# Optimization experiments

Hardware: AMD Instinct MI355X
Metric: run time of the kernel (lower is better)

## Reference

```python
import jax, jax.numpy as jnp
import numpy as np

H = 512      # LSTM hidden size (hard-coded in BiLstm)
ATT = 20     # attention size
EPS = 1e-5


def _ln(x, gamma, beta):
    mu = x.mean(-1, keepdims=True)
    var = x.var(-1, keepdims=True)
    return (x - mu) / jnp.sqrt(var + EPS) * gamma + beta


def _bn(x, gamma, beta):
    # BatchNorm1d in training mode: x [B, C, T], stats over (batch, time)
    mu = x.mean((0, 2), keepdims=True)
    var = x.var((0, 2), keepdims=True)
    return (x - mu) / jnp.sqrt(var + EPS) * gamma[None, :, None] + beta[None, :, None]


def _lstm_dir(x_seq, w_ih, w_hh, g_gamma, g_beta, c_gamma, c_beta, reverse):
    # x_seq: [T, B, in] ; w_ih: [4H, in] ; w_hh: [4H, H]
    T, B, _ = x_seq.shape
    xp = jnp.einsum('tbi,gi->tbg', x_seq, w_ih)  # precompute input projections [T,B,4H]
    gg = g_gamma.reshape(4, H)
    gb = g_beta.reshape(4, H)

    def step(carry, xt):
        h, c = carry
        pre = xt + h @ w_hh.T                    # [B, 4H]
        pre = _ln(pre.reshape(B, 4, H), gg, gb)  # per-gate LayerNorm
        i, f, g, o = pre[:, 0], pre[:, 1], pre[:, 2], pre[:, 3]
        c = jax.nn.sigmoid(f) * c + jax.nn.sigmoid(i) * jnp.tanh(g)
        h = jax.nn.sigmoid(o) * jnp.tanh(_ln(c, c_gamma, c_beta))
        return (h, c), h

    init = (jnp.zeros((B, H), x_seq.dtype), jnp.zeros((B, H), x_seq.dtype))
    _, hs = jax.lax.scan(step, init, xp, reverse=reverse)
    return hs  # [T, B, H], time-ordered


def _bilstm_layer(x_seq, w_ih, w_hh, gg, gb, cg, cb):
    fwd = _lstm_dir(x_seq, w_ih[0], w_hh[0], gg[0], gb[0], cg[0], cb[0], False)
    bwd = _lstm_dir(x_seq, w_ih[1], w_hh[1], gg[1], gb[1], cg[1], cb[1], True)
    return jnp.concatenate([fwd, bwd], axis=-1)  # [T, B, 2H]


def setup_inputs() -> dict:
    key = jax.random.key(0)
    ks = jax.random.split(key, 12)
    B, T, V = 32, 512, 128
    d = {}
    d['x'] = jax.random.normal(ks[0], (B, T, V), jnp.float32)
    # BatchNorm params
    d['bn1_gamma'] = jnp.ones((V,), jnp.float32)
    d['bn1_beta'] = jnp.zeros((V,), jnp.float32)
    d['bn2_gamma'] = jnp.ones((2 * H,), jnp.float32)
    d['bn2_beta'] = jnp.zeros((2 * H,), jnp.float32)
    # Layer 0 (input V), layer 1 (input 2H); 2 directions stacked on axis 0
    d['w_ih0'] = jax.random.normal(ks[1], (2, 4 * H, V), jnp.float32) * 0.05
    d['w_hh0'] = jax.random.normal(ks[2], (2, 4 * H, H), jnp.float32) * 0.05
    d['g_gamma0'] = jnp.ones((2, 4 * H), jnp.float32)
    d['g_beta0'] = jnp.zeros((2, 4 * H), jnp.float32)
    d['c_gamma0'] = jnp.ones((2, H), jnp.float32)
    d['c_beta0'] = jnp.zeros((2, H), jnp.float32)
    d['w_ih1'] = jax.random.normal(ks[3], (2, 4 * H, 2 * H), jnp.float32) * 0.05
    d['w_hh1'] = jax.random.normal(ks[4], (2, 4 * H, H), jnp.float32) * 0.05
    d['g_gamma1'] = jnp.ones((2, 4 * H), jnp.float32)
    d['g_beta1'] = jnp.zeros((2, 4 * H), jnp.float32)
    d['c_gamma1'] = jnp.ones((2, H), jnp.float32)
    d['c_beta1'] = jnp.zeros((2, H), jnp.float32)
    # Attention params
    d['w_omega'] = jax.random.normal(ks[5], (2 * H, ATT), jnp.float32) * 0.05
    d['b_omega'] = jax.random.normal(ks[6], (ATT,), jnp.float32) * 0.05
    d['u_omega'] = jax.random.normal(ks[7], (ATT,), jnp.float32) * 0.05
    return d


def reference(x, bn1_gamma, bn1_beta, bn2_gamma, bn2_beta,
              w_ih0, w_hh0, g_gamma0, g_beta0, c_gamma0, c_beta0,
              w_ih1, w_hh1, g_gamma1, g_beta1, c_gamma1, c_beta1,
              w_omega, b_omega, u_omega):
    # x: [B, T, V]; dropout layers are identity (eval)
    h = jnp.transpose(x, (0, 2, 1))              # [B, V, T]
    h = _bn(h, bn1_gamma, bn1_beta)
    h = jnp.transpose(h, (2, 0, 1))              # [T, B, V]
    h = _bilstm_layer(h, w_ih0, w_hh0, g_gamma0, g_beta0, c_gamma0, c_beta0)
    h = _bilstm_layer(h, w_ih1, w_hh1, g_gamma1, g_beta1, c_gamma1, c_beta1)
    h = jnp.transpose(h, (1, 2, 0))              # [B, 2H, T]
    h = _bn(h, bn2_gamma, bn2_beta)
    h = jnp.transpose(h, (0, 2, 1))              # [B, T, 2H]
    # Additive attention pooling
    v = jnp.tanh(h @ w_omega + b_omega)          # [B, T, ATT]
    vu = v @ u_omega                             # [B, T]
    alphas = jax.nn.softmax(vu, axis=1)
    out = jnp.sum(h * alphas[..., None], axis=1)  # [B, 2H]
    return out
```

## Files before the change

kernel.cpp:

```cpp
#include <hip/hip_runtime.h>
#include <hip/hip_bf16.h>

#define LN_EPS 1e-5f

typedef __attribute__((ext_vector_type(4))) float    f32x4;
typedef __attribute__((ext_vector_type(8))) short    s16x8;
typedef __attribute__((ext_vector_type(8))) _Float16 f16x8;
typedef __attribute__((ext_vector_type(4))) unsigned u32x4;

__device__ __forceinline__ float sigmoidf_(float x){ return 1.0f/(1.0f+expf(-x)); }

__device__ __forceinline__ float fsig(float x){
  return 1.0f/(1.0f + __expf(-x));
}
__device__ __forceinline__ float ftanh(float x){
  float xx = fminf(fmaxf(x, -15.f), 15.f);
  float e = __expf(2.f*xx);
  return (e - 1.f)/(e + 1.f);
}

__device__ __forceinline__ short bf16_hi_bits(float f){
  __hip_bfloat16 h = __float2bfloat16(f);
  return *reinterpret_cast<short*>(&h);
}
__device__ __forceinline__ float bf16_hi_val(float f){
  return __bfloat162float(__float2bfloat16(f));
}

__device__ __forceinline__ float agent_load_f(const float* p){
  return __hip_atomic_load((float*)p, __ATOMIC_RELAXED, __HIP_MEMORY_SCOPE_AGENT);
}
__device__ __forceinline__ void agent_store_f(float* p, float v){
  __hip_atomic_store(p, v, __ATOMIC_RELAXED, __HIP_MEMORY_SCOPE_AGENT);
}

__global__ void k_bn1_stats(const float* __restrict__ x, float* __restrict__ stats){
  int tid = threadIdx.x;
  int cg = tid >> 3, ro = tid & 7;
  int c4 = cg * 4;
  float s[4] = {0,0,0,0}, q[4] = {0,0,0,0};
  int rbase = blockIdx.x * 64;
  for (int i = 0; i < 8; ++i){
    int row = rbase + i*8 + ro;
    f32x4 v = *(const f32x4*)(x + (size_t)row*128 + c4);
    #pragma unroll
    for (int e=0;e<4;e++){ s[e]+=v[e]; q[e]+=v[e]*v[e]; }
  }
  #pragma unroll
  for (int o=1;o<8;o<<=1){
    #pragma unroll
    for (int e=0;e<4;e++){ s[e]+=__shfl_xor(s[e],o); q[e]+=__shfl_xor(q[e],o); }
  }
  if (ro==0){
    #pragma unroll
    for (int e=0;e<4;e++){
      atomicAdd(&stats[c4+e], s[e]);
      atomicAdd(&stats[128+c4+e], q[e]);
    }
  }
}

__global__ void k_bn1_fin(const float* __restrict__ stats, const float* __restrict__ gamma,
                          const float* __restrict__ beta, float* __restrict__ ss){
  int c = threadIdx.x;
  if (c < 128){
    float N = 16384.0f;
    float mean = stats[c]/N;
    float var  = stats[128+c]/N - mean*mean;
    float scale = gamma[c] * rsqrtf(var + LN_EPS);
    ss[c] = scale;
    ss[128+c] = beta[c] - mean*scale;
  }
}

__global__ void k_cvt_split(const float* __restrict__ s, __hip_bfloat16* __restrict__ hi,
                            __hip_bfloat16* __restrict__ lo, int n){
  for (int i = blockIdx.x*blockDim.x + threadIdx.x; i < n; i += gridDim.x*blockDim.x){
    float v = s[i];
    __hip_bfloat16 h = __float2bfloat16(v);
    hi[i] = h;
    lo[i] = __float2bfloat16(v - __bfloat162float(h));
  }
}

__global__ void k_pack_whh(const float* __restrict__ whh, _Float16* __restrict__ wpk){
  size_t i = (size_t)blockIdx.x*256 + threadIdx.x;
  int k = (int)(i & 511);
  size_t ci = i >> 9;
  int col = (int)(ci & 2047);
  int dirr = (int)(ci >> 11);
  int gate = col >> 9, cig = col & 511, c16 = cig >> 4, lc = cig & 15;
  int kt = k >> 5, ksub = k & 31, hi = ksub >> 3, j = ksub & 7;
  size_t dst = ((((size_t)(dirr*4+gate)*16 + kt)*32 + c16)*64 + (hi*16+lc))*8 + j;
  wpk[dst] = (_Float16)whh[i];
}

__global__ __launch_bounds__(256) void gemm_split(const float* __restrict__ A,
                                                  const __hip_bfloat16* __restrict__ Bhi,
                                                  const __hip_bfloat16* __restrict__ Blo,
                                                  _Float16* __restrict__ C,
                                                  int M, int N, int K,
                                                  int a_mode, const float* __restrict__ ss){
  __shared__ __align__(16) __hip_bfloat16 Ah[128*32];
  __shared__ __align__(16) __hip_bfloat16 Al[128*32];
  __shared__ __align__(16) __hip_bfloat16 Bh[128*32];
  __shared__ __align__(16) __hip_bfloat16 Bl[128*32];
  int n0 = blockIdx.x * 128, m0 = blockIdx.y * 128;
  int tid = threadIdx.x, lane = tid & 63, wave = tid >> 6;
  int wm = wave >> 1, wn = wave & 1;
  f32x4 acc[4][4] = {};
  int r = tid >> 2, sseg = tid & 3;
  for (int kt = 0; kt < K; kt += 32){
    #pragma unroll
    for (int half = 0; half < 2; ++half){
      int m = m0 + half*64 + r;
      const float* src;
      if (a_mode){
        int t = m >> 5, b = m & 31;
        src = A + ((size_t)(b*512 + t))*128 + kt + sseg*8;
      } else {
        src = A + (size_t)m*K + kt + sseg*8;
      }
      f32x4 v0 = *(const f32x4*)src;
      f32x4 v1 = *(const f32x4*)(src + 4);
      s16x8 vh, vl;
      #pragma unroll
      for (int e=0;e<4;e++){
        float f0 = v0[e], f1 = v1[e];
        if (a_mode){
          int k = kt + sseg*8;
          f0 = f0*ss[k+e]   + ss[128+k+e];
          f1 = f1*ss[k+4+e] + ss[128+k+4+e];
        }
        float h0 = bf16_hi_val(f0), h1 = bf16_hi_val(f1);
        vh[e]   = bf16_hi_bits(f0); vl[e]   = bf16_hi_bits(f0 - h0);
        vh[4+e] = bf16_hi_bits(f1); vl[4+e] = bf16_hi_bits(f1 - h1);
      }
      *(s16x8*)&Ah[(half*64+r)*32 + sseg*8] = vh;
      *(s16x8*)&Al[(half*64+r)*32 + sseg*8] = vl;
      u32x4 bh = *(const u32x4*)(Bhi + (size_t)(n0 + half*64 + r)*K + kt + sseg*8);
      u32x4 bl = *(const u32x4*)(Blo + (size_t)(n0 + half*64 + r)*K + kt + sseg*8);
      *(u32x4*)&Bh[(half*64+r)*32 + sseg*8] = bh;
      *(u32x4*)&Bl[(half*64+r)*32 + sseg*8] = bl;
    }
    __syncthreads();
    s16x8 afh[4], afl[4], bfh[4], bfl[4];
    int k8 = (lane >> 4) * 8;
    int ra = wm*64 + (lane & 15), rb = wn*64 + (lane & 15);
    #pragma unroll
    for (int mi=0;mi<4;mi++){
      afh[mi] = *(const s16x8*)&Ah[(ra + mi*16)*32 + k8];
      afl[mi] = *(const s16x8*)&Al[(ra + mi*16)*32 + k8];
    }
    #pragma unroll
    for (int ni=0;ni<4;ni++){
      bfh[ni] = *(const s16x8*)&Bh[(rb + ni*16)*32 + k8];
      bfl[ni] = *(const s16x8*)&Bl[(rb + ni*16)*32 + k8];
    }
    #pragma unroll
    for (int mi=0;mi<4;mi++)
      #pragma unroll
      for (int ni=0;ni<4;ni++){
        acc[mi][ni] = __builtin_amdgcn_mfma_f32_16x16x32_bf16(afh[mi], bfh[ni], acc[mi][ni], 0, 0, 0);
        acc[mi][ni] = __builtin_amdgcn_mfma_f32_16x16x32_bf16(afl[mi], bfh[ni], acc[mi][ni], 0, 0, 0);
        acc[mi][ni] = __builtin_amdgcn_mfma_f32_16x16x32_bf16(afh[mi], bfl[ni], acc[mi][ni], 0, 0, 0);
      }
    __syncthreads();
  }
  #pragma unroll
  for (int mi=0;mi<4;mi++)
    #pragma unroll
    for (int ni=0;ni<4;ni++){
      int col  = n0 + wn*64 + ni*16 + (lane & 15);
      int row0 = m0 + wm*64 + mi*16 + (lane >> 4)*4;
      #pragma unroll
      for (int rr=0;rr<4;rr++)
        C[(size_t)(row0+rr)*N + col] = (_Float16)acc[mi][ni][rr];
    }
}

#define CHUNK 516

__global__ __launch_bounds__(512, 1) void lstm_fast(
    const _Float16* __restrict__ xp,
    const _Float16* __restrict__ wpk,
    const float* __restrict__ gg, const float* __restrict__ gb,
    const float* __restrict__ cgam, const float* __restrict__ cbet,
    float* __restrict__ out,
    float* __restrict__ tf,
    unsigned* __restrict__ flags)
{
  int blk = blockIdx.x;
  int sub = blk & 15;
  int bq = blk >> 4;
  int dir = sub >> 3, gate = (sub >> 1) & 3, half = sub & 1;
  int tid = threadIdx.x, lane = tid & 63, wv = tid >> 6;
  int b0 = bq * 2;
  int grp = bq*2 + dir;
  int blkbase = (bq << 4) | (dir << 3);
  int own_sub = gate*2 + half;

  __shared__ __align__(16) _Float16 hfrag[16*64*8];
  __shared__ float c_s[2][512];
  __shared__ float red[8][2][2];
  __shared__ float redc[8][2][2];
  __shared__ float lnstat[8][2];

  for (int i = tid; i < 16*64*8; i += 512) hfrag[i] = (_Float16)0.f;
  for (int i = tid; i < 2*512;  i += 512) c_s[i>>9][i&511] = 0.f;
  __syncthreads();

  int j = tid;
  float g0s = gg[dir*2048 + j],        g0b = gb[dir*2048 + j];
  float g1s = gg[dir*2048 + 512 + j],  g1b = gb[dir*2048 + 512 + j];
  float g2s = gg[dir*2048 + 1024 + j], g2b = gb[dir*2048 + 1024 + j];
  float g3s = gg[dir*2048 + 1536 + j], g3b = gb[dir*2048 + 1536 + j];
  float cgv = cgam[dir*512 + j],       cbv = cbet[dir*512 + j];

  const _Float16* wbase = wpk + (size_t)(dir*4 + gate) * (16*32*64*8);
  int c16a = half*16 + wv*2, c16b = c16a + 1;
  f16x8 wA[16], wB[16];
  #pragma unroll
  for (int kt = 0; kt < 16; ++kt){
    wA[kt] = *(const f16x8*)&wbase[(((size_t)kt*32 + c16a)*64 + lane)*8];
    wB[kt] = *(const f16x8*)&wbase[(((size_t)kt*32 + c16b)*64 + lane)*8];
  }

  for (int t = 0; t < 512; ++t){
    asm volatile("" : "+v"(wA[0]), "+v"(wA[1]), "+v"(wA[2]), "+v"(wA[3]),
                      "+v"(wA[4]), "+v"(wA[5]), "+v"(wA[6]), "+v"(wA[7]));
    asm volatile("" : "+v"(wA[8]), "+v"(wA[9]), "+v"(wA[10]), "+v"(wA[11]),
                      "+v"(wA[12]), "+v"(wA[13]), "+v"(wA[14]), "+v"(wA[15]));
    asm volatile("" : "+v"(wB[0]), "+v"(wB[1]), "+v"(wB[2]), "+v"(wB[3]),
                      "+v"(wB[4]), "+v"(wB[5]), "+v"(wB[6]), "+v"(wB[7]));
    asm volatile("" : "+v"(wB[8]), "+v"(wB[9]), "+v"(wB[10]), "+v"(wB[11]),
                      "+v"(wB[12]), "+v"(wB[13]), "+v"(wB[14]), "+v"(wB[15]));
    int pos = dir ? (511 - t) : t;
    int buf = t & 1;
    float xv0[2], xv1[2];
    if (lane < 16){
      const _Float16* xb = xp + (size_t)(pos*32 + b0)*4096 + dir*2048 + gate*512 + half*256;
      #pragma unroll
      for (int r = 0; r < 2; ++r){
        xv0[r] = (float)xb[(size_t)r*4096 + (wv*2)*16 + lane];
        xv1[r] = (float)xb[(size_t)r*4096 + (wv*2)*16 + lane + 16];
      }
    }
    f32x4 acc0 = {}, acc1 = {};
    #pragma unroll
    for (int kt = 0; kt < 16; ++kt){
      f16x8 afrag = *(const f16x8*)&hfrag[(kt*64 + lane)*8];
      acc0 = __builtin_amdgcn_mfma_f32_16x16x32_f16(afrag, wA[kt], acc0, 0, 0, 0);
      acc1 = __builtin_amdgcn_mfma_f32_16x16x32_f16(afrag, wB[kt], acc1, 0, 0, 0);
    }
    float* chk = tf + ((size_t)(grp*2 + buf)*8 + own_sub)*CHUNK;
    float s[2] = {0,0}, q[2] = {0,0};
    if (lane < 16){
      int cA = (wv*2)*16 + lane, cB = cA + 16;
      #pragma unroll
      for (int r = 0; r < 2; ++r){
        float v0 = acc0[r] + xv0[r];
        float v1 = acc1[r] + xv1[r];
        agent_store_f(chk + r*256 + cA, v0);
        agent_store_f(chk + r*256 + cB, v1);
        s[r] = v0 + v1; q[r] = v0*v0 + v1*v1;
      }
    }
    #pragma unroll
    for (int o = 1; o < 16; o <<= 1){
      #pragma unroll
      for (int r = 0; r < 2; ++r){ s[r] += __shfl_xor(s[r], o); q[r] += __shfl_xor(q[r], o); }
    }
    if (lane == 0){
      #pragma unroll
      for (int r = 0; r < 2; ++r){ red[wv][r][0] = s[r]; red[wv][r][1] = q[r]; }
    }
    __syncthreads();
    if (tid < 4){
      int b = tid >> 1, wh = tid & 1;
      float S = 0.f;
      #pragma unroll
      for (int w8 = 0; w8 < 8; ++w8) S += red[w8][b][wh];
      agent_store_f(chk + 512 + b*2 + wh, S);
    }
    asm volatile("s_waitcnt vmcnt(0)" ::: "memory");
    __syncthreads();
    if (tid == 0)
      __hip_atomic_store(&flags[blk*64], (unsigned)(t+1), __ATOMIC_RELAXED, __HIP_MEMORY_SCOPE_AGENT);
    if (tid < 7){
      int idx = tid < own_sub ? tid : tid + 1;
      int sblk = blkbase + idx;
      while (__hip_atomic_load(&flags[sblk*64], __ATOMIC_RELAXED, __HIP_MEMORY_SCOPE_AGENT)
             < (unsigned)(t+1)){ }
    }
    __syncthreads();
    const float* gbase = tf + ((size_t)(grp*2 + buf)*8)*CHUNK;
    int hf = j >> 8, cc = j & 255;
    float p[4][2];
    #pragma unroll
    for (int g = 0; g < 4; ++g){
      const float* cp = gbase + (size_t)(g*2 + hf)*CHUNK + cc;
      #pragma unroll
      for (int b = 0; b < 2; ++b) p[g][b] = agent_load_f(cp + b*256);
    }
    if (tid < 8){
      int g = tid >> 1, b = tid & 1;
      float S = 0.f, Q = 0.f;
      #pragma unroll
      for (int hh = 0; hh < 2; ++hh){
        S += agent_load_f(gbase + (size_t)(g*2 + hh)*CHUNK + 512 + b*2);
        Q += agent_load_f(gbase + (size_t)(g*2 + hh)*CHUNK + 512 + b*2 + 1);
      }
      float mean = S*(1.0f/512.0f);
      float var  = Q*(1.0f/512.0f) - mean*mean;
      lnstat[tid][0] = mean; lnstat[tid][1] = rsqrtf(var + LN_EPS);
    }
    __syncthreads();
    float cs[2], cq2[2], ov[2], cnv[2];
    #pragma unroll
    for (int b = 0; b < 2; ++b){
      float pi = (p[0][b] - lnstat[0*2+b][0])*lnstat[0*2+b][1]*g0s + g0b;
      float pf = (p[1][b] - lnstat[1*2+b][0])*lnstat[1*2+b][1]*g1s + g1b;
      float pv = (p[2][b] - lnstat[2*2+b][0])*lnstat[2*2+b][1]*g2s + g2b;
      ov[b]    = (p[3][b] - lnstat[3*2+b][0])*lnstat[3*2+b][1]*g3s + g3b;
      float cn = fsig(pf)*c_s[b][j] + fsig(pi)*ftanh(pv);
      c_s[b][j] = cn; cnv[b] = cn;
      cs[b] = cn; cq2[b] = cn*cn;
    }
    #pragma unroll
    for (int o = 1; o < 64; o <<= 1){
      #pragma unroll
      for (int b = 0; b < 2; ++b){ cs[b] += __shfl_xor(cs[b], o); cq2[b] += __shfl_xor(cq2[b], o); }
    }
    if (lane == 0){
      #pragma unroll
      for (int b = 0; b < 2; ++b){ redc[wv][b][0] = cs[b]; redc[wv][b][1] = cq2[b]; }
    }
    __syncthreads();
    #pragma unroll
    for (int b = 0; b < 2; ++b){
      float S = 0.f, Q = 0.f;
      #pragma unroll
      for (int w8 = 0; w8 < 8; ++w8){ S += redc[w8][b][0]; Q += redc[w8][b][1]; }
      float mean = S*(1.0f/512.0f);
      float var  = Q*(1.0f/512.0f) - mean*mean;
      float rstd = rsqrtf(var + LN_EPS);
      float cl = (cnv[b] - mean)*rstd*cgv + cbv;
      float hv = fsig(ov[b]) * ftanh(cl);
      hfrag[(((j >> 5)*64) + ((j & 31) >> 3)*16 + b)*8 + (j & 7)] = (_Float16)hv;
      if (own_sub == 0)
        out[(size_t)(pos*32 + b0 + b)*1024 + dir*512 + j] = hv;
    }
    __syncthreads();
  }
}

__global__ void k_bn2_stats(const float* __restrict__ h1, float* __restrict__ stats){
  int tid = threadIdx.x;
  int c4 = tid*4;
  float s[4]={0,0,0,0}, q[4]={0,0,0,0};
  int rbase = blockIdx.x*64;
  for (int i=0;i<64;i++){
    f32x4 v = *(const f32x4*)(h1 + (size_t)(rbase+i)*1024 + c4);
    #pragma unroll
    for (int e=0;e<4;e++){ s[e]+=v[e]; q[e]+=v[e]*v[e]; }
  }
  #pragma unroll
  for (int e=0;e<4;e++){
    atomicAdd(&stats[c4+e], s[e]);
    atomicAdd(&stats[1024+c4+e], q[e]);
  }
}

__global__ void k_bn2_fin(const float* __restrict__ stats, const float* __restrict__ gamma,
                          const float* __restrict__ beta, float* __restrict__ ss){
  int c = blockIdx.x*256 + threadIdx.x;
  if (c < 1024){
    float N = 16384.0f;
    float mean = stats[c]/N;
    float var  = stats[1024+c]/N - mean*mean;
    float scale = gamma[c] * rsqrtf(var + LN_EPS);
    ss[c] = scale;
    ss[1024+c] = beta[c] - mean*scale;
  }
}

__global__ void k_att1(const float* __restrict__ h1, const float* __restrict__ ss,
                       const float* __restrict__ wom, const float* __restrict__ bom,
                       const float* __restrict__ uom, float* __restrict__ vu){
  __shared__ float tmp[4][64];
  int tid = threadIdx.x, wave = tid >> 6, ln = tid & 63;
  int part = ln/20, a = ln - part*20;
  bool active = (part < 3);
  for (int rr = 0; rr < 4; ++rr){
    int row = blockIdx.x*16 + wave*4 + rr;
    float acc = 0.0f;
    if (active){
      int n0 = part*342, n1 = (part==2) ? 1024 : (n0+342);
      for (int n = n0; n < n1; ++n){
        float hv = h1[(size_t)row*1024 + n]*ss[n] + ss[1024+n];
        acc += hv * wom[n*20 + a];
      }
    }
    tmp[wave][ln] = acc;
    __syncthreads();
    float pv = 0.0f;
    if (ln < 20){
      float v = tanhf(tmp[wave][ln] + tmp[wave][ln+20] + tmp[wave][ln+40] + bom[ln]);
      pv = v*uom[ln];
    }
    #pragma unroll
    for (int o=1;o<32;o<<=1) pv += __shfl_xor(pv, o);
    if (ln == 0) vu[row] = pv;
    __syncthreads();
  }
}

__global__ void k_att3(const float* __restrict__ h1, const float* __restrict__ ss,
                       const float* __restrict__ vu, float* __restrict__ out){
  __shared__ float al[512];
  __shared__ float red[4];
  int tid = threadIdx.x;
  int b = blockIdx.x >> 3, ch = blockIdx.x & 7;
  for (int t = tid; t < 512; t += 128) al[t] = vu[t*32 + b];
  __syncthreads();
  float m = -1e30f;
  for (int t = tid; t < 512; t += 128) m = fmaxf(m, al[t]);
  #pragma unroll
  for (int o=1;o<64;o<<=1) m = fmaxf(m, __shfl_xor(m,o));
  if ((tid & 63) == 0) red[tid>>6] = m;
  __syncthreads();
  m = fmaxf(red[0], red[1]);
  float s = 0.0f;
  for (int t = tid; t < 512; t += 128){ float e = expf(al[t]-m); al[t] = e; s += e; }
  #pragma unroll
  for (int o=1;o<64;o<<=1) s += __shfl_xor(s,o);
  if ((tid & 63) == 0) red[2 + (tid>>6)] = s;
  __syncthreads();
  float inv = 1.0f / (red[2] + red[3]);
  int n = ch*128 + tid;
  float acc = 0.0f;
  #pragma unroll 4
  for (int t = 0; t < 512; ++t) acc += al[t]*h1[(size_t)(t*32+b)*1024 + n];
  out[b*1024 + n] = acc*inv*ss[n] + ss[1024+n];
}

extern "C" void kernel_launch(void* const* d_in, const int* in_sizes, int n_in,
                              void* d_out, int out_size, void* d_ws, size_t ws_size,
                              hipStream_t stream){
  const float* x    = (const float*)d_in[0];
  const float* bn1g = (const float*)d_in[1];
  const float* bn1b = (const float*)d_in[2];
  const float* bn2g = (const float*)d_in[3];
  const float* bn2b = (const float*)d_in[4];
  const float* wih0 = (const float*)d_in[5];
  const float* whh0 = (const float*)d_in[6];
  const float* gg0  = (const float*)d_in[7];
  const float* gb0  = (const float*)d_in[8];
  const float* cg0  = (const float*)d_in[9];
  const float* cb0  = (const float*)d_in[10];
  const float* wih1 = (const float*)d_in[11];
  const float* whh1 = (const float*)d_in[12];
  const float* gg1  = (const float*)d_in[13];
  const float* gb1  = (const float*)d_in[14];
  const float* cg1  = (const float*)d_in[15];
  const float* cb1  = (const float*)d_in[16];
  const float* wom  = (const float*)d_in[17];
  const float* bom  = (const float*)d_in[18];
  const float* uom  = (const float*)d_in[19];
  float* out = (float*)d_out;

  char* w = (char*)d_ws;
  size_t off = 0;
  auto take = [&](size_t bytes)->void*{
    void* p = w + off;
    off += (bytes + 255) & ~(size_t)255;
    return p;
  };
  _Float16* xp = (_Float16*)take(16384ull*4096*2);
  float* hA = (float*)take(16384ull*1024*4);
  __hip_bfloat16* w0hi = (__hip_bfloat16*)take(4096ull*128*2);
  __hip_bfloat16* w0lo = (__hip_bfloat16*)take(4096ull*128*2);
  __hip_bfloat16* w1hi = (__hip_bfloat16*)take(4096ull*1024*2);
  __hip_bfloat16* w1lo = (__hip_bfloat16*)take(4096ull*1024*2);
  _Float16* wpk0 = (_Float16*)take(2ull*2048*512*2);
  _Float16* wpk1 = (_Float16*)take(2ull*2048*512*2);
  float* tilesf = (float*)take(32ull*2*8*CHUNK*4);
  unsigned* flags = (unsigned*)take(256ull*64*4);
  float* stats1 = (float*)take(256*4);
  float* ss1    = (float*)take(256*4);
  float* stats2 = (float*)take(2048*4);
  float* ss2    = (float*)take(2048*4);
  float* vu     = (float*)take(16384ull*4);
  (void)ws_size; (void)in_sizes; (void)n_in; (void)out_size;

  hipMemsetAsync(stats1, 0, 256*4, stream);
  hipMemsetAsync(stats2, 0, 2048*4, stream);

  k_bn1_stats<<<256,256,0,stream>>>(x, stats1);
  k_bn1_fin<<<1,128,0,stream>>>(stats1, bn1g, bn1b, ss1);
  k_cvt_split<<<256,256,0,stream>>>(wih0, w0hi, w0lo, 4096*128);
  k_cvt_split<<<2048,256,0,stream>>>(wih1, w1hi, w1lo, 4096*1024);
  k_pack_whh<<<8192,256,0,stream>>>(whh0, wpk0);
  k_pack_whh<<<8192,256,0,stream>>>(whh1, wpk1);

  gemm_split<<<dim3(32,128),256,0,stream>>>(x, w0hi, w0lo, xp, 16384, 4096, 128, 1, ss1);

  hipMemsetAsync(flags, 0, 256*64*4, stream);
  lstm_fast<<<256,512,0,stream>>>(xp, wpk0, gg0, gb0, cg0, cb0, hA, tilesf, flags);

  gemm_split<<<dim3(32,128),256,0,stream>>>(hA, w1hi, w1lo, xp, 16384, 4096, 1024, 0, nullptr);

  hipMemsetAsync(flags, 0, 256*64*4, stream);
  lstm_fast<<<256,512,0,stream>>>(xp, wpk1, gg1, gb1, cg1, cb1, hA, tilesf, flags);

  k_bn2_stats<<<256,256,0,stream>>>(hA, stats2);
  k_bn2_fin<<<4,256,0,stream>>>(stats2, bn2g, bn2b, ss2);
  k_att1<<<1024,256,0,stream>>>(hA, ss2, wom, bom, uom, vu);
  k_att3<<<256,128,0,stream>>>(hA, ss2, vu, out);
}
```

Before: 5.575 ms.

## Use single fp16 MFMA for input projections and trim LSTM step synchronisation

The input-projection GEMM drops its three-pass bf16 hi/lo split and does one fp16 MFMA pass, which removes two thirds of the matrix work and half the staging traffic. In the LSTM step, the block-wide barrier before the flag publish becomes a per-wave atomic increment, with the spin threshold scaled to 8 waves per step. Each thread now recomputes the LayerNorm statistics itself instead of having a few threads compute them into shared memory behind an extra barrier. The cost is lower GEMM precision (fp16 with an 11-bit mantissa instead of roughly 16 bits from the split), more redundant global loads per thread, and more atomic traffic on the flags.

New measurement: 5.923 ms. 6.2% more time.

```diff
diff --git a/kernel.cpp b/kernel.cpp
--- a/kernel.cpp
+++ b/kernel.cpp
@@ -4,11 +4,8 @@
 #define LN_EPS 1e-5f
 
 typedef __attribute__((ext_vector_type(4))) float    f32x4;
-typedef __attribute__((ext_vector_type(8))) short    s16x8;
 typedef __attribute__((ext_vector_type(8))) _Float16 f16x8;
 typedef __attribute__((ext_vector_type(4))) unsigned u32x4;
-
-__device__ __forceinline__ float sigmoidf_(float x){ return 1.0f/(1.0f+expf(-x)); }
 
 __device__ __forceinline__ float fsig(float x){
   return 1.0f/(1.0f + __expf(-x));
@@ -17,14 +14,6 @@
   float xx = fminf(fmaxf(x, -15.f), 15.f);
   float e = __expf(2.f*xx);
   return (e - 1.f)/(e + 1.f);
-}
-
-__device__ __forceinline__ short bf16_hi_bits(float f){
-  __hip_bfloat16 h = __float2bfloat16(f);
-  return *reinterpret_cast<short*>(&h);
-}
-__device__ __forceinline__ float bf16_hi_val(float f){
-  return __bfloat162float(__float2bfloat16(f));
 }
 
 __device__ __forceinline__ float agent_load_f(const float* p){
@@ -73,14 +62,9 @@
   }
 }
 
-__global__ void k_cvt_split(const float* __restrict__ s, __hip_bfloat16* __restrict__ hi,
-                            __hip_bfloat16* __restrict__ lo, int n){
-  for (int i = blockIdx.x*blockDim.x + threadIdx.x; i < n; i += gridDim.x*blockDim.x){
-    float v = s[i];
-    __hip_bfloat16 h = __float2bfloat16(v);
-    hi[i] = h;
-    lo[i] = __float2bfloat16(v - __bfloat162float(h));
-  }
+__global__ void k_cvt_f16(const float* __restrict__ s, _Float16* __restrict__ d, int n){
+  for (int i = blockIdx.x*blockDim.x + threadIdx.x; i < n; i += gridDim.x*blockDim.x)
+    d[i] = (_Float16)s[i];
 }
 
 __global__ void k_pack_whh(const float* __restrict__ whh, _Float16* __restrict__ wpk){
@@ -95,16 +79,13 @@
   wpk[dst] = (_Float16)whh[i];
 }
 
-__global__ __launch_bounds__(256) void gemm_split(const float* __restrict__ A,
-                                                  const __hip_bfloat16* __restrict__ Bhi,
-                                                  const __hip_bfloat16* __restrict__ Blo,
-                                                  _Float16* __restrict__ C,
-                                                  int M, int N, int K,
-                                                  int a_mode, const float* __restrict__ ss){
-  __shared__ __align__(16) __hip_bfloat16 Ah[128*32];
-  __shared__ __align__(16) __hip_bfloat16 Al[128*32];
-  __shared__ __align__(16) __hip_bfloat16 Bh[128*32];
-  __shared__ __align__(16) __hip_bfloat16 Bl[128*32];
+__global__ __launch_bounds__(256) void gemm_f16(const float* __restrict__ A,
+                                                const _Float16* __restrict__ Bp,
+                                                _Float16* __restrict__ C,
+                                                int M, int N, int K,
+                                                int a_mode, const float* __restrict__ ss){
+  __shared__ __align__(16) _Float16 As[128*32];
+  __shared__ __align__(16) _Float16 Bs[128*32];
   int n0 = blockIdx.x * 128, m0 = blockIdx.y * 128;
   int tid = threadIdx.x, lane = tid & 63, wave = tid >> 6;
   int wm = wave >> 1, wn = wave & 1;
@@ -123,7 +104,7 @@
       }
       f32x4 v0 = *(const f32x4*)src;
       f32x4 v1 = *(const f32x4*)(src + 4);
-      s16x8 vh, vl;
+      f16x8 vh;
       #pragma unroll
       for (int e=0;e<4;e++){
         float f0 = v0[e], f1 = v1[e];
@@ -132,39 +113,25 @@
           f0 = f0*ss[k+e]   + ss[128+k+e];
           f1 = f1*ss[k+4+e] + ss[128+k+4+e];
         }
-        float h0 = bf16_hi_val(f0), h1 = bf16_hi_val(f1);
-        vh[e]   = bf16_hi_bits(f0); vl[e]   = bf16_hi_bits(f0 - h0);
-        vh[4+e] = bf16_hi_bits(f1); vl[4+e] = bf16_hi_bits(f1 - h1);
-      }
-      *(s16x8*)&Ah[(half*64+r)*32 + sseg*8] = vh;
-      *(s16x8*)&Al[(half*64+r)*32 + sseg*8] = vl;
-      u32x4 bh = *(const u32x4*)(Bhi + (size_t)(n0 + half*64 + r)*K + kt + sseg*8);
-      u32x4 bl = *(const u32x4*)(Blo + (size_t)(n0 + half*64 + r)*K + kt + sseg*8);
-      *(u32x4*)&Bh[(half*64+r)*32 + sseg*8] = bh;
-      *(u32x4*)&Bl[(half*64+r)*32 + sseg*8] = bl;
-    }
-    __syncthreads();
-    s16x8 afh[4], afl[4], bfh[4], bfl[4];
+        vh[e] = (_Float16)f0; vh[4+e] = (_Float16)f1;
+      }
+      *(f16x8*)&As[(half*64+r)*32 + sseg*8] = vh;
+      u32x4 bv = *(const u32x4*)(Bp + (size_t)(n0 + half*64 + r)*K + kt + sseg*8);
+      *(u32x4*)&Bs[(half*64+r)*32 + sseg*8] = bv;
+    }
+    __syncthreads();
+    f16x8 af[4], bf[4];
     int k8 = (lane >> 4) * 8;
     int ra = wm*64 + (lane & 15), rb = wn*64 + (lane & 15);
     #pragma unroll
-    for (int mi=0;mi<4;mi++){
-      afh[mi] = *(const s16x8*)&Ah[(ra + mi*16)*32 + k8];
-      afl[mi] = *(const s16x8*)&Al[(ra + mi*16)*32 + k8];
-    }
-    #pragma unroll
-    for (int ni=0;ni<4;ni++){
-      bfh[ni] = *(const s16x8*)&Bh[(rb + ni*16)*32 + k8];
-      bfl[ni] = *(const s16x8*)&Bl[(rb + ni*16)*32 + k8];
-    }
+    for (int mi=0;mi<4;mi++) af[mi] = *(const f16x8*)&As[(ra + mi*16)*32 + k8];
+    #pragma unroll
+    for (int ni=0;ni<4;ni++) bf[ni] = *(const f16x8*)&Bs[(rb + ni*16)*32 + k8];
     #pragma unroll
     for (int mi=0;mi<4;mi++)
       #pragma unroll
-      for (int ni=0;ni<4;ni++){
-        acc[mi][ni] = __builtin_amdgcn_mfma_f32_16x16x32_bf16(afh[mi], bfh[ni], acc[mi][ni], 0, 0, 0);
-        acc[mi][ni] = __builtin_amdgcn_mfma_f32_16x16x32_bf16(afl[mi], bfh[ni], acc[mi][ni], 0, 0, 0);
-        acc[mi][ni] = __builtin_amdgcn_mfma_f32_16x16x32_bf16(afh[mi], bfl[ni], acc[mi][ni], 0, 0, 0);
-      }
+      for (int ni=0;ni<4;ni++)
+        acc[mi][ni] = __builtin_amdgcn_mfma_f32_16x16x32_f16(af[mi], bf[ni], acc[mi][ni], 0, 0, 0);
     __syncthreads();
   }
   #pragma unroll
@@ -204,7 +171,6 @@
   __shared__ float c_s[2][512];
   __shared__ float red[8][2][2];
   __shared__ float redc[8][2][2];
-  __shared__ float lnstat[8][2];
 
   for (int i = tid; i < 16*64*8; i += 512) hfrag[i] = (_Float16)0.f;
   for (int i = tid; i < 2*512;  i += 512) c_s[i>>9][i&511] = 0.f;
@@ -284,14 +250,13 @@
       agent_store_f(chk + 512 + b*2 + wh, S);
     }
     asm volatile("s_waitcnt vmcnt(0)" ::: "memory");
-    __syncthreads();
-    if (tid == 0)
-      __hip_atomic_store(&flags[blk*64], (unsigned)(t+1), __ATOMIC_RELAXED, __HIP_MEMORY_SCOPE_AGENT);
+    if (lane == 0)
+      __hip_atomic_fetch_add(&flags[blk*64], 1u, __ATOMIC_RELAXED, __HIP_MEMORY_SCOPE_AGENT);
     if (tid < 7){
       int idx = tid < own_sub ? tid : tid + 1;
       int sblk = blkbase + idx;
       while (__hip_atomic_load(&flags[sblk*64], __ATOMIC_RELAXED, __HIP_MEMORY_SCOPE_AGENT)
-             < (unsigned)(t+1)){ }
+             < (unsigned)(8*(t+1))){ }
     }
     __syncthreads();
     const float* gbase = tf + ((size_t)(grp*2 + buf)*8)*CHUNK;
@@ -303,26 +268,26 @@
       #pragma unroll
       for (int b = 0; b < 2; ++b) p[g][b] = agent_load_f(cp + b*256);
     }
-    if (tid < 8){
-      int g = tid >> 1, b = tid & 1;
-      float S = 0.f, Q = 0.f;
-      #pragma unroll
-      for (int hh = 0; hh < 2; ++hh){
-        S += agent_load_f(gbase + (size_t)(g*2 + hh)*CHUNK + 512 + b*2);
-        Q += agent_load_f(gbase + (size_t)(g*2 + hh)*CHUNK + 512 + b*2 + 1);
-      }
-      float mean = S*(1.0f/512.0f);
-      float var  = Q*(1.0f/512.0f) - mean*mean;
-      lnstat[tid][0] = mean; lnstat[tid][1] = rsqrtf(var + LN_EPS);
-    }
-    __syncthreads();
+    float mu[4][2], rs[4][2];
+    #pragma unroll
+    for (int g = 0; g < 4; ++g)
+      #pragma unroll
+      for (int b = 0; b < 2; ++b){
+        float S = agent_load_f(gbase + (size_t)(g*2+0)*CHUNK + 512 + b*2)
+                + agent_load_f(gbase + (size_t)(g*2+1)*CHUNK + 512 + b*2);
+        float Q = agent_load_f(gbase + (size_t)(g*2+0)*CHUNK + 512 + b*2 + 1)
+                + agent_load_f(gbase + (size_t)(g*2+1)*CHUNK + 512 + b*2 + 1);
+        float mean = S*(1.0f/512.0f);
+        float var  = Q*(1.0f/512.0f) - mean*mean;
+        mu[g][b] = mean; rs[g][b] = rsqrtf(var + LN_EPS);
+      }
     float cs[2], cq2[2], ov[2], cnv[2];
     #pragma unroll
     for (int b = 0; b < 2; ++b){
-      float pi = (p[0][b] - lnstat[0*2+b][0])*lnstat[0*2+b][1]*g0s + g0b;
-      float pf = (p[1][b] - lnstat[1*2+b][0])*lnstat[1*2+b][1]*g1s + g1b;
-      float pv = (p[2][b] - lnstat[2*2+b][0])*lnstat[2*2+b][1]*g2s + g2b;
-      ov[b]    = (p[3][b] - lnstat[3*2+b][0])*lnstat[3*2+b][1]*g3s + g3b;
+      float pi = (p[0][b] - mu[0][b])*rs[0][b]*g0s + g0b;
+      float pf = (p[1][b] - mu[1][b])*rs[1][b]*g1s + g1b;
+      float pv = (p[2][b] - mu[2][b])*rs[2][b]*g2s + g2b;
+      ov[b]    = (p[3][b] - mu[3][b])*rs[3][b]*g3s + g3b;
       float cn = fsig(pf)*c_s[b][j] + fsig(pi)*ftanh(pv);
       c_s[b][j] = cn; cnv[b] = cn;
       cs[b] = cn; cq2[b] = cn*cn;
@@ -479,10 +444,8 @@
   };
   _Float16* xp = (_Float16*)take(16384ull*4096*2);
   float* hA = (float*)take(16384ull*1024*4);
-  __hip_bfloat16* w0hi = (__hip_bfloat16*)take(4096ull*128*2);
-  __hip_bfloat16* w0lo = (__hip_bfloat16*)take(4096ull*128*2);
-  __hip_bfloat16* w1hi = (__hip_bfloat16*)take(4096ull*1024*2);
-  __hip_bfloat16* w1lo = (__hip_bfloat16*)take(4096ull*1024*2);
+  _Float16* w0h = (_Float16*)take(4096ull*128*2);
+  _Float16* w1h = (_Float16*)take(4096ull*1024*2);
   _Float16* wpk0 = (_Float16*)take(2ull*2048*512*2);
   _Float16* wpk1 = (_Float16*)take(2ull*2048*512*2);
   float* tilesf = (float*)take(32ull*2*8*CHUNK*4);
@@ -499,17 +462,17 @@
 
   k_bn1_stats<<<256,256,0,stream>>>(x, stats1);
   k_bn1_fin<<<1,128,0,stream>>>(stats1, bn1g, bn1b, ss1);
-  k_cvt_split<<<256,256,0,stream>>>(wih0, w0hi, w0lo, 4096*128);
-  k_cvt_split<<<2048,256,0,stream>>>(wih1, w1hi, w1lo, 4096*1024);
+  k_cvt_f16<<<256,256,0,stream>>>(wih0, w0h, 4096*128);
+  k_cvt_f16<<<2048,256,0,stream>>>(wih1, w1h, 4096*1024);
   k_pack_whh<<<8192,256,0,stream>>>(whh0, wpk0);
   k_pack_whh<<<8192,256,0,stream>>>(whh1, wpk1);
 
-  gemm_split<<<dim3(32,128),256,0,stream>>>(x, w0hi, w0lo, xp, 16384, 4096, 128, 1, ss1);
+  gemm_f16<<<dim3(32,128),256,0,stream>>>(x, w0h, xp, 16384, 4096, 128, 1, ss1);
 
   hipMemsetAsync(flags, 0, 256*64*4, stream);
   lstm_fast<<<256,512,0,stream>>>(xp, wpk0, gg0, gb0, cg0, cb0, hA, tilesf, flags);
 
-  gemm_split<<<dim3(32,128),256,0,stream>>>(hA, w1hi, w1lo, xp, 16384, 4096, 1024, 0, nullptr);
+  gemm_f16<<<dim3(32,128),256,0,stream>>>(hA, w1h, xp, 16384, 4096, 1024, 0, nullptr);
 
   hipMemsetAsync(flags, 0, 256*64*4, stream);
   lstm_fast<<<256,512,0,stream>>>(xp, wpk1, gg1, gb1, cg1, cb1, hA, tilesf, flags);
```
